# Optimization experiments

Measured on AMD Instinct MI355X. Metric: run time of the kernel, lower is better.

## Reference

```python
import jax, jax.numpy as jnp
import numpy as np

CUTOFF = 10.0
EPS_W = 1e-5
EPS_LN = 1e-5

def _silu(v):
    return v * jax.nn.sigmoid(v)

def setup_inputs() -> dict:
    key = jax.random.key(0)
    ks = jax.random.split(key, 12)
    N, E, H, R = 50000, 300000, 256, 64
    s = lambda fan_in: 1.0 / np.sqrt(fan_in)
    inp = {
        'x': jax.random.normal(ks[0], (N, H), jnp.float32),
        'edge_index': jax.random.randint(ks[1], (2, E), 0, N, jnp.int64 if jax.config.jax_enable_x64 else jnp.int32),
        'distances': jax.random.uniform(ks[2], (E,), jnp.float32) * CUTOFF,
        'centers': jnp.linspace(0.0, CUTOFF, R).astype(jnp.float32),
        'widths': jnp.full((R,), CUTOFF / R, jnp.float32),
        'rbf_w1': jax.random.normal(ks[3], (R, R), jnp.float32) * s(R),
        'rbf_b1': jnp.zeros((R,), jnp.float32),
        'rbf_w2': jax.random.normal(ks[4], (R, R), jnp.float32) * s(R),
        'rbf_b2': jnp.zeros((R,), jnp.float32),
        'filt_w1': jax.random.normal(ks[5], (R, H), jnp.float32) * s(R),
        'filt_b1': jnp.zeros((H,), jnp.float32),
        'filt_w2': jax.random.normal(ks[6], (H, H), jnp.float32) * s(H),
        'filt_b2': jnp.zeros((H,), jnp.float32),
        'filt_w3': jax.random.normal(ks[7], (H, H), jnp.float32) * s(H),
        'filt_b3': jnp.zeros((H,), jnp.float32),
        'node_w': jax.random.normal(ks[8], (H, H), jnp.float32) * s(H),
        'node_b': jnp.zeros((H,), jnp.float32),
        'ln_g': jnp.ones((H,), jnp.float32),
        'ln_b': jnp.zeros((H,), jnp.float32),
        'gate_w': jax.random.normal(ks[9], (H, H), jnp.float32) * s(H),
        'gate_b': jnp.zeros((H,), jnp.float32),
    }
    return inp

def reference(x, edge_index, distances, centers, widths,
              rbf_w1, rbf_b1, rbf_w2, rbf_b2,
              filt_w1, filt_b1, filt_w2, filt_b2, filt_w3, filt_b3,
              node_w, node_b, ln_g, ln_b, gate_w, gate_b):
    # LearnableRBF: envelope * gaussian basis, then 2-layer SiLU proj
    d = distances
    env = 0.5 * (jnp.cos(d * jnp.pi / CUTOFF) + 1.0) * (d < CUTOFF).astype(x.dtype)  # [E]
    rbf = jnp.exp(-0.5 * ((d[:, None] - centers) / (jnp.abs(widths) + EPS_W)) ** 2)   # [E,R]
    r = rbf * env[:, None]
    r = _silu(r @ rbf_w1 + rbf_b1) @ rbf_w2 + rbf_b2                                  # [E,R]
    # filter network: Lin-SiLU-Lin-SiLU-Lin
    W = _silu(r @ filt_w1 + filt_b1)
    W = _silu(W @ filt_w2 + filt_b2) @ filt_w3 + filt_b3                              # [E,H]
    # gather -> modulate -> scatter-add (CFConv messaging)
    row, col = edge_index[0], edge_index[1]
    msg = (x[col] @ node_w + node_b) * W                                              # [E,H]
    agg = jax.ops.segment_sum(msg, row, num_segments=x.shape[0])                      # [N,H]
    h = x + agg
    mu = jnp.mean(h, axis=-1, keepdims=True)
    var = jnp.var(h, axis=-1, keepdims=True)
    out = (h - mu) / jnp.sqrt(var + EPS_LN) * ln_g + ln_b
    return out * jax.nn.sigmoid(out @ gate_w + gate_b)
```

## Files before the change

kernel.cpp:

```cpp
#include <hip/hip_runtime.h>
#include <hip/hip_bf16.h>
#include <math.h>

typedef __attribute__((ext_vector_type(8))) short bf16x8;
typedef __attribute__((ext_vector_type(4))) float f32x4;
typedef unsigned short ushort_t;

constexpr float F_CUTOFF = 10.0f;
constexpr float F_EPS_W  = 1e-5f;
constexpr float F_EPS_LN = 1e-5f;
constexpr float F_PI     = 3.14159265358979323846f;

__device__ __forceinline__ float silu_f(float v)   { return v / (1.0f + __expf(-v)); }
__device__ __forceinline__ float sigmoid_f(float v){ return 1.0f / (1.0f + __expf(-v)); }

__device__ __forceinline__ ushort_t f2bf(float f) {
    union { __hip_bfloat16 h; ushort_t u; } v; v.h = __float2bfloat16(f); return v.u;
}
__device__ __forceinline__ float bf2f(ushort_t u) {
    union { unsigned u; float f; } v; v.u = ((unsigned)u) << 16; return v.f;
}

__global__ void count_kernel(const int* __restrict__ eidx, int* __restrict__ cnt, int E)
{
    int e = blockIdx.x * 256 + threadIdx.x;
    if (e < E) atomicAdd(&cnt[eidx[e]], 1);
}

__global__ __launch_bounds__(256)
void scan_sum_kernel(const int* __restrict__ cnt, int* __restrict__ part, int N, int range)
{
    __shared__ int red[256];
    int base = blockIdx.x * range;
    int s = 0;
    for (int i = threadIdx.x; i < range; i += 256) {
        int idx = base + i;
        if (idx < N) s += cnt[idx];
    }
    red[threadIdx.x] = s;
    __syncthreads();
    #pragma unroll
    for (int o = 128; o > 0; o >>= 1) {
        if (threadIdx.x < o) red[threadIdx.x] += red[threadIdx.x + o];
        __syncthreads();
    }
    if (threadIdx.x == 0) part[blockIdx.x] = red[0];
}

__global__ __launch_bounds__(256)
void scan_write_kernel(const int* __restrict__ part, int* __restrict__ cnt ,
                       int* __restrict__ start, int N, int range, int E)
{
    __shared__ int ex[256];
    int tid = threadIdx.x;
    int v = part[tid];
    ex[tid] = v;
    __syncthreads();
    for (int o = 1; o < 256; o <<= 1) {
        int add = (tid >= o) ? ex[tid - o] : 0;
        __syncthreads();
        ex[tid] += add;
        __syncthreads();
    }
    int run = ex[tid] - v;
    int base = tid * range;
    for (int i = 0; i < range; ++i) {
        int idx = base + i;
        if (idx < N) {
            int c = cnt[idx];
            start[idx] = run;
            cnt[idx] = run;
            run += c;
        }
    }
    if (tid == 0) start[N] = E;
}

__global__ void scatter_kernel(const int* __restrict__ eidx, const float* __restrict__ dist,
                               int* __restrict__ cursor,
                               int* __restrict__ colp, int* __restrict__ nodep,
                               float* __restrict__ distp, int E)
{
    int e = blockIdx.x * 256 + threadIdx.x;
    if (e < E) {
        int row = eidx[e];
        int s = atomicAdd(&cursor[row], 1);
        colp[s]  = eidx[E + e];
        nodep[s] = row;
        distp[s] = dist[e];
    }
}

__global__ void cvt_transpose_kernel(const float* __restrict__ in, ushort_t* __restrict__ out,
                                     int K, int N, int logK)
{
    int idx = blockIdx.x * 256 + threadIdx.x;
    if (idx >= K * N) return;
    int n = idx >> logK;
    int k = idx & (K - 1);
    out[idx] = f2bf(in[k * N + n]);
}

__global__ void combine_w_kernel(const float* __restrict__ w2, const float* __restrict__ fw1,
                                 ushort_t* __restrict__ out)
{
    int idx = blockIdx.x * 256 + threadIdx.x;
    int c = idx >> 6, j = idx & 63;
    float s = 0.f;
    #pragma unroll 8
    for (int n = 0; n < 64; ++n) s += w2[j * 64 + n] * fw1[n * 256 + c];
    out[idx] = f2bf(s);
}

__global__ void combine_b_kernel(const float* __restrict__ b2, const float* __restrict__ fw1,
                                 const float* __restrict__ fb1, float* __restrict__ out)
{
    int c = threadIdx.x;
    float s = fb1[c];
    #pragma unroll 8
    for (int n = 0; n < 64; ++n) s += b2[n] * fw1[n * 256 + c];
    out[c] = s;
}

__global__ __launch_bounds__(256)
void gemm256_bf16_kernel(const float* __restrict__ A, const float* __restrict__ Wm,
                         const float* __restrict__ bias, ushort_t* __restrict__ out, int M)
{
    __shared__ float4 As4[64][64];
    const int t = threadIdx.x;
    const int row0 = blockIdx.x * 64;

    #pragma unroll
    for (int i = 0; i < 16; ++i) {
        int flat = t + i * 256;
        int r = flat >> 6, k4 = flat & 63;
        int row = row0 + r;
        float4 v = make_float4(0.f, 0.f, 0.f, 0.f);
        if (row < M) v = reinterpret_cast<const float4*>(A)[row * 64 + k4];
        As4[r][k4] = v;
    }
    __syncthreads();

    const int jt  = t & 31;
    const int et  = t >> 5;
    const int j04 = jt * 2;
    const int r0  = et * 8;

    float acc[8][8];
    #pragma unroll
    for (int r = 0; r < 8; ++r)
        #pragma unroll
        for (int c = 0; c < 8; ++c) acc[r][c] = 0.f;

    for (int k4 = 0; k4 < 64; ++k4) {
        float4 a4[8];
        #pragma unroll
        for (int r = 0; r < 8; ++r) a4[r] = As4[r0 + r][k4];
        #pragma unroll
        for (int q = 0; q < 4; ++q) {
            const int k = k4 * 4 + q;
            float4 b0 = reinterpret_cast<const float4*>(Wm)[k * 64 + j04];
            float4 b1 = reinterpret_cast<const float4*>(Wm)[k * 64 + j04 + 1];
            float bb[8] = {b0.x, b0.y, b0.z, b0.w, b1.x, b1.y, b1.z, b1.w};
            float av;
            #pragma unroll
            for (int r = 0; r < 8; ++r) {
                av = (q == 0) ? a4[r].x : (q == 1) ? a4[r].y : (q == 2) ? a4[r].z : a4[r].w;
                #pragma unroll
                for (int c = 0; c < 8; ++c) acc[r][c] = fmaf(av, bb[c], acc[r][c]);
            }
        }
    }

    float4 bv0 = reinterpret_cast<const float4*>(bias)[j04];
    float4 bv1 = reinterpret_cast<const float4*>(bias)[j04 + 1];
    float bb[8] = {bv0.x, bv0.y, bv0.z, bv0.w, bv1.x, bv1.y, bv1.z, bv1.w};

    #pragma unroll
    for (int r = 0; r < 8; ++r) {
        int row = row0 + r0 + r;
        if (row >= M) continue;
        ushort_t o8[8];
        #pragma unroll
        for (int c = 0; c < 8; ++c) o8[c] = f2bf(acc[r][c] + bb[c]);
        *reinterpret_cast<uint4*>(out + (size_t)row * 256 + jt * 8) = *reinterpret_cast<uint4*>(o8);
    }
}

__global__ __launch_bounds__(256)
void gate_gemm_kernel(const float* __restrict__ A, const float* __restrict__ Wm,
                      const float* __restrict__ bias, float* __restrict__ out, int M)
{
    __shared__ float4 As4[64][64];
    const int t = threadIdx.x;
    const int row0 = blockIdx.x * 64;

    #pragma unroll
    for (int i = 0; i < 16; ++i) {
        int flat = t + i * 256;
        int r = flat >> 6, k4 = flat & 63;
        int row = row0 + r;
        float4 v = make_float4(0.f, 0.f, 0.f, 0.f);
        if (row < M) v = reinterpret_cast<const float4*>(A)[row * 64 + k4];
        As4[r][k4] = v;
    }
    __syncthreads();

    const int jt  = t & 31;
    const int et  = t >> 5;
    const int j04 = jt * 2;
    const int r0  = et * 8;

    float acc[8][8];
    #pragma unroll
    for (int r = 0; r < 8; ++r)
        #pragma unroll
        for (int c = 0; c < 8; ++c) acc[r][c] = 0.f;

    for (int k4 = 0; k4 < 64; ++k4) {
        float4 a4[8];
        #pragma unroll
        for (int r = 0; r < 8; ++r) a4[r] = As4[r0 + r][k4];
        #pragma unroll
        for (int q = 0; q < 4; ++q) {
            const int k = k4 * 4 + q;
            float4 b0 = reinterpret_cast<const float4*>(Wm)[k * 64 + j04];
            float4 b1 = reinterpret_cast<const float4*>(Wm)[k * 64 + j04 + 1];
            float bb[8] = {b0.x, b0.y, b0.z, b0.w, b1.x, b1.y, b1.z, b1.w};
            float av;
            #pragma unroll
            for (int r = 0; r < 8; ++r) {
                av = (q == 0) ? a4[r].x : (q == 1) ? a4[r].y : (q == 2) ? a4[r].z : a4[r].w;
                #pragma unroll
                for (int c = 0; c < 8; ++c) acc[r][c] = fmaf(av, bb[c], acc[r][c]);
            }
        }
    }

    float4 bv0 = reinterpret_cast<const float4*>(bias)[j04];
    float4 bv1 = reinterpret_cast<const float4*>(bias)[j04 + 1];
    float bb[8] = {bv0.x, bv0.y, bv0.z, bv0.w, bv1.x, bv1.y, bv1.z, bv1.w};

    #pragma unroll
    for (int r = 0; r < 8; ++r) {
        int row = row0 + r0 + r;
        if (row >= M) continue;
        float4 a0 = As4[r0 + r][j04];
        float4 a1 = As4[r0 + r][j04 + 1];
        float aa[8] = {a0.x, a0.y, a0.z, a0.w, a1.x, a1.y, a1.z, a1.w};
        float o[8];
        #pragma unroll
        for (int c = 0; c < 8; ++c) o[c] = aa[c] * sigmoid_f(acc[r][c] + bb[c]);
        reinterpret_cast<float4*>(out)[row * 64 + j04]     = make_float4(o[0], o[1], o[2], o[3]);
        reinterpret_cast<float4*>(out)[row * 64 + j04 + 1] = make_float4(o[4], o[5], o[6], o[7]);
    }
}

__global__ __launch_bounds__(256)
void rbf_kernel(const float* __restrict__ distp,
                const float* __restrict__ centers, const float* __restrict__ widths,
                ushort_t* __restrict__ r, int Mc)
{
    int idx = blockIdx.x * 256 + threadIdx.x;
    if (idx >= Mc * 8) return;
    int e  = idx >> 3;
    int c0 = (idx & 7) * 8;
    float d = distp[e];
    float env = (d < F_CUTOFF) ? 0.5f * (__cosf(d * (F_PI / F_CUTOFF)) + 1.0f) : 0.0f;
    ushort_t o[8];
    #pragma unroll
    for (int i = 0; i < 8; ++i) {
        int n = c0 + i;
        float w = fabsf(widths[n]) + F_EPS_W;
        float z = (d - centers[n]) / w;
        o[i] = f2bf(env * __expf(-0.5f * z * z));
    }
    *reinterpret_cast<uint4*>(r + (size_t)e * 64 + c0) = *reinterpret_cast<uint4*>(o);
}

__global__ __launch_bounds__(256, 4)
void gemm_k64_kernel(const ushort_t* A, const ushort_t* __restrict__ Wt,
                     const float* __restrict__ bias, ushort_t* out, int M)
{
    __shared__ __align__(16) unsigned char sA[128 * 128];
    const int t = threadIdx.x;
    const int m0 = blockIdx.x * 128;
    const int w = t >> 6, lane = t & 63;
    const int g = lane >> 4, q = lane & 15;

    #pragma unroll
    for (int i = 0; i < 4; ++i) {
        int s = t + i * 256;
        int r = s >> 3, u = s & 7;
        int row = m0 + r; row = (row < M) ? row : (M - 1);
        uint4 v = *reinterpret_cast<const uint4*>(A + (size_t)row * 64 + ((u ^ (r & 7)) * 8));
        *reinterpret_cast<uint4*>(sA + s * 16) = v;
    }
    __syncthreads();

    f32x4 acc[2][4];
    #pragma unroll
    for (int mt = 0; mt < 2; ++mt)
        #pragma unroll
        for (int nt = 0; nt < 4; ++nt) acc[mt][nt] = (f32x4){0.f, 0.f, 0.f, 0.f};

    #pragma unroll
    for (int kk = 0; kk < 2; ++kk) {
        bf16x8 b[4];
        #pragma unroll
        for (int nt = 0; nt < 4; ++nt) {
            int n = nt * 16 + q;
            b[nt] = *reinterpret_cast<const bf16x8*>(Wt + n * 64 + kk * 32 + g * 8);
        }
        bf16x8 a[2];
        #pragma unroll
        for (int mt = 0; mt < 2; ++mt) {
            int m = w * 32 + mt * 16 + q;
            int unit = (4 * kk + g) ^ (m & 7);
            a[mt] = *reinterpret_cast<const bf16x8*>(sA + m * 128 + unit * 16);
        }
        #pragma unroll
        for (int mt = 0; mt < 2; ++mt)
            #pragma unroll
            for (int nt = 0; nt < 4; ++nt)
                acc[mt][nt] = __builtin_amdgcn_mfma_f32_16x16x32_bf16(a[mt], b[nt], acc[mt][nt], 0, 0, 0);
    }
    __syncthreads();

    const bool evenq = (q & 1) == 0;
    #pragma unroll
    for (int nt = 0; nt < 4; ++nt) {
        int n0  = nt * 16 + q;
        int n_e = n0 & ~1;
        float2 bv = *reinterpret_cast<const float2*>(bias + n_e);
        #pragma unroll
        for (int mt = 0; mt < 2; ++mt) {
            float v[4], p[4];
            #pragma unroll
            for (int r = 0; r < 4; ++r) { v[r] = acc[mt][nt][r]; p[r] = __shfl_xor(v[r], 1, 64); }
            #pragma unroll
            for (int rr = 0; rr < 2; ++rr) {
                int r = evenq ? rr : (2 + rr);
                float lo = silu_f((evenq ? v[r] : p[r]) + bv.x);
                float hi = silu_f((evenq ? p[r] : v[r]) + bv.y);
                int m = w * 32 + mt * 16 + 4 * g + r;
                unsigned u = (unsigned)f2bf(lo) | ((unsigned)f2bf(hi) << 16);
                *reinterpret_cast<unsigned*>(sA + m * 128 + n_e * 2) = u;
            }
        }
    }
    __syncthreads();

    {
        int row = t >> 1, j = t & 1;
        if (m0 + row < M) {
            #pragma unroll
            for (int i = 0; i < 4; ++i) {
                uint4 v = *reinterpret_cast<const uint4*>(sA + row * 128 + (j * 4 + i) * 16);
                *reinterpret_cast<uint4*>(out + (size_t)(m0 + row) * 64 + (j * 4 + i) * 8) = v;
            }
        }
    }
}

__global__ __launch_bounds__(256, 4)
void gemm_k64n256_kernel(const ushort_t* __restrict__ A, const ushort_t* __restrict__ Wt,
                         const float* __restrict__ bias, ushort_t* __restrict__ out, int M)
{
    __shared__ __align__(16) unsigned char sA[64 * 128];
    __shared__ __align__(16) unsigned char obuf[32 * 512];
    const int t = threadIdx.x;
    const int m0 = blockIdx.x * 64;
    const int wn = t >> 6, lane = t & 63;
    const int g = lane >> 4, q = lane & 15;

    #pragma unroll
    for (int i = 0; i < 2; ++i) {
        int s = t + i * 256;
        int r = s >> 3, u = s & 7;
        int row = m0 + r; row = (row < M) ? row : (M - 1);
        uint4 v = *reinterpret_cast<const uint4*>(A + (size_t)row * 64 + ((u ^ (r & 7)) * 8));
        *reinterpret_cast<uint4*>(sA + s * 16) = v;
    }
    __syncthreads();

    f32x4 acc[4][4];
    #pragma unroll
    for (int mt = 0; mt < 4; ++mt)
        #pragma unroll
        for (int nt = 0; nt < 4; ++nt) acc[mt][nt] = (f32x4){0.f, 0.f, 0.f, 0.f};

    #pragma unroll
    for (int kk = 0; kk < 2; ++kk) {
        bf16x8 b[4];
        #pragma unroll
        for (int nt = 0; nt < 4; ++nt) {
            int n = wn * 64 + nt * 16 + q;
            b[nt] = *reinterpret_cast<const bf16x8*>(Wt + n * 64 + kk * 32 + g * 8);
        }
        bf16x8 a[4];
        #pragma unroll
        for (int mt = 0; mt < 4; ++mt) {
            int m = mt * 16 + q;
            int unit = (4 * kk + g) ^ (m & 7);
            a[mt] = *reinterpret_cast<const bf16x8*>(sA + m * 128 + unit * 16);
        }
        #pragma unroll
        for (int mt = 0; mt < 4; ++mt)
            #pragma unroll
            for (int nt = 0; nt < 4; ++nt)
                acc[mt][nt] = __builtin_amdgcn_mfma_f32_16x16x32_bf16(a[mt], b[nt], acc[mt][nt], 0, 0, 0);
    }

    const bool evenq = (q & 1) == 0;
    #pragma unroll
    for (int half = 0; half < 2; ++half) {
        #pragma unroll
        for (int mtl = 0; mtl < 2; ++mtl) {
            int mt = half * 2 + mtl;
            #pragma unroll
            for (int nt = 0; nt < 4; ++nt) {
                int n0  = wn * 64 + nt * 16 + q;
                int n_e = n0 & ~1;
                float2 bv = *reinterpret_cast<const float2*>(bias + n_e);
                float v[4], p[4];
                #pragma unroll
                for (int r = 0; r < 4; ++r) { v[r] = acc[mt][nt][r]; p[r] = __shfl_xor(v[r], 1, 64); }
                #pragma unroll
                for (int rr = 0; rr < 2; ++rr) {
                    int r = evenq ? rr : (2 + rr);
                    float lo = silu_f((evenq ? v[r] : p[r]) + bv.x);
                    float hi = silu_f((evenq ? p[r] : v[r]) + bv.y);
                    int ml = mtl * 16 + 4 * g + r;
                    unsigned u = (unsigned)f2bf(lo) | ((unsigned)f2bf(hi) << 16);
                    *reinterpret_cast<unsigned*>(obuf + ml * 512 + n_e * 2) = u;
                }
            }
        }
        __syncthreads();
        {
            int row = t >> 3, c = t & 7;
            int grow = m0 + half * 32 + row;
            if (grow < M) {
                #pragma unroll
                for (int i = 0; i < 4; ++i) {
                    uint4 v = *reinterpret_cast<const uint4*>(obuf + row * 512 + (c + 8 * i) * 16);
                    *reinterpret_cast<uint4*>(out + (size_t)grow * 256 + (c + 8 * i) * 8) = v;
                }
            }
        }
        __syncthreads();
    }
}

__global__ __launch_bounds__(256, 3)
void fused_de_kernel(const ushort_t* A, const ushort_t* __restrict__ Wt2,
                     const float* __restrict__ b2,
                     const ushort_t* __restrict__ Wt3, const float* __restrict__ b3,
                     ushort_t* out, int M)
{
    __shared__ __align__(16) unsigned char sbuf[2][8192];
    __shared__ __align__(16) unsigned char f2l[64 * 512];

    const int t  = threadIdx.x;
    const int m0 = blockIdx.x * 64;
    const int wn   = t >> 6;
    const int lane = t & 63;
    const int g = lane >> 4, q = lane & 15;

    const int s0r = t >> 3,         s0u = t & 7;
    const int s1r = (t + 256) >> 3, s1u = t & 7;
    const ushort_t* src0base = A + (size_t)((m0 + s0r < M) ? (m0 + s0r) : (M - 1)) * 256 + ((s0u ^ (s0r & 7)) * 8);
    const ushort_t* src1base = A + (size_t)((m0 + s1r < M) ? (m0 + s1r) : (M - 1)) * 256 + ((s1u ^ (s1r & 7)) * 8);

    uint4 p0 = *reinterpret_cast<const uint4*>(src0base);
    uint4 p1 = *reinterpret_cast<const uint4*>(src1base);
    *reinterpret_cast<uint4*>(&sbuf[0][t * 16])         = p0;
    *reinterpret_cast<uint4*>(&sbuf[0][(t + 256) * 16]) = p1;
    __syncthreads();

    f32x4 acc[4][4];
    #pragma unroll
    for (int mt = 0; mt < 4; ++mt)
        #pragma unroll
        for (int nt = 0; nt < 4; ++nt) acc[mt][nt] = (f32x4){0.f, 0.f, 0.f, 0.f};

    for (int kt = 0; kt < 4; ++kt) {
        const int cur = kt & 1;
        uint4 nx0, nx1;
        if (kt < 3) {
            nx0 = *reinterpret_cast<const uint4*>(src0base + (kt + 1) * 64);
            nx1 = *reinterpret_cast<const uint4*>(src1base + (kt + 1) * 64);
        }
        #pragma unroll
        for (int ks = 0; ks < 2; ++ks) {
            bf16x8 b[4];
            #pragma unroll
            for (int nt = 0; nt < 4; ++nt) {
                int n = wn * 64 + nt * 16 + q;
                b[nt] = *reinterpret_cast<const bf16x8*>(Wt2 + (size_t)n * 256 + kt * 64 + ks * 32 + g * 8);
            }
            bf16x8 a[4];
            #pragma unroll
            for (int mt = 0; mt < 4; ++mt) {
                int r = mt * 16 + q;
                int u = (ks * 4 + g) ^ (r & 7);
                a[mt] = *reinterpret_cast<const bf16x8*>(&sbuf[cur][r * 128 + u * 16]);
            }
            #pragma unroll
            for (int mt = 0; mt < 4; ++mt)
                #pragma unroll
                for (int nt = 0; nt < 4; ++nt)
                    acc[mt][nt] = __builtin_amdgcn_mfma_f32_16x16x32_bf16(a[mt], b[nt], acc[mt][nt], 0, 0, 0);
        }
        __syncthreads();
        if (kt < 3) {
            *reinterpret_cast<uint4*>(&sbuf[cur ^ 1][t * 16])         = nx0;
            *reinterpret_cast<uint4*>(&sbuf[cur ^ 1][(t + 256) * 16]) = nx1;
            __syncthreads();
        }
    }

    const bool evenq = (q & 1) == 0;
    #pragma unroll
    for (int nt = 0; nt < 4; ++nt) {
        int n0  = wn * 64 + nt * 16 + q;
        int n_e = n0 & ~1;
        float2 bv = *reinterpret_cast<const float2*>(b2 + n_e);
        #pragma unroll
        for (int mt = 0; mt < 4; ++mt) {
            float v[4], p[4];
            #pragma unroll
            for (int r = 0; r < 4; ++r) { v[r] = acc[mt][nt][r]; p[r] = __shfl_xor(v[r], 1, 64); }
            #pragma unroll
            for (int rr = 0; rr < 2; ++rr) {
                int r = evenq ? rr : (2 + rr);
                float lo = silu_f((evenq ? v[r] : p[r]) + bv.x);
                float hi = silu_f((evenq ? p[r] : v[r]) + bv.y);
                int m = mt * 16 + 4 * g + r;
                unsigned u = (unsigned)f2bf(lo) | ((unsigned)f2bf(hi) << 16);
                int byte = m * 512 + (((n_e >> 3) ^ (m & 7)) << 4) + ((n_e & 7) * 2);
                *reinterpret_cast<unsigned*>(f2l + byte) = u;
            }
        }
    }
    __syncthreads();

    #pragma unroll
    for (int mt = 0; mt < 4; ++mt)
        #pragma unroll
        for (int nt = 0; nt < 4; ++nt) acc[mt][nt] = (f32x4){0.f, 0.f, 0.f, 0.f};

    #pragma unroll
    for (int kk = 0; kk < 8; ++kk) {
        bf16x8 b[4];
        #pragma unroll
        for (int nt = 0; nt < 4; ++nt) {
            int n = wn * 64 + nt * 16 + q;
            b[nt] = *reinterpret_cast<const bf16x8*>(Wt3 + (size_t)n * 256 + kk * 32 + g * 8);
        }
        bf16x8 a[4];
        #pragma unroll
        for (int mt = 0; mt < 4; ++mt) {
            int m = mt * 16 + q;
            int unit = (4 * kk + g) ^ (m & 7);
            a[mt] = *reinterpret_cast<const bf16x8*>(f2l + m * 512 + unit * 16);
        }
        #pragma unroll
        for (int mt = 0; mt < 4; ++mt)
            #pragma unroll
            for (int nt = 0; nt < 4; ++nt)
                acc[mt][nt] = __builtin_amdgcn_mfma_f32_16x16x32_bf16(a[mt], b[nt], acc[mt][nt], 0, 0, 0);
    }

    unsigned char* obuf = &sbuf[0][0];
    #pragma unroll
    for (int half = 0; half < 2; ++half) {
        __syncthreads();
        #pragma unroll
        for (int mtl = 0; mtl < 2; ++mtl) {
            int mt = half * 2 + mtl;
            #pragma unroll
            for (int nt = 0; nt < 4; ++nt) {
                int n0  = wn * 64 + nt * 16 + q;
                int n_e = n0 & ~1;
                float2 bv = *reinterpret_cast<const float2*>(b3 + n_e);
                float v[4], p[4];
                #pragma unroll
                for (int r = 0; r < 4; ++r) { v[r] = acc[mt][nt][r]; p[r] = __shfl_xor(v[r], 1, 64); }
                #pragma unroll
                for (int rr = 0; rr < 2; ++rr) {
                    int r = evenq ? rr : (2 + rr);
                    float lo = (evenq ? v[r] : p[r]) + bv.x;
                    float hi = (evenq ? p[r] : v[r]) + bv.y;
                    int ml = mtl * 16 + 4 * g + r;
                    unsigned u = (unsigned)f2bf(lo) | ((unsigned)f2bf(hi) << 16);
                    *reinterpret_cast<unsigned*>(obuf + ml * 512 + n_e * 2) = u;
                }
            }
        }
        __syncthreads();
        {
            int row = t >> 3, c = t & 7;
            int grow = m0 + half * 32 + row;
            if (grow < M) {
                #pragma unroll
                for (int i = 0; i < 4; ++i) {
                    uint4 v = *reinterpret_cast<const uint4*>(obuf + row * 512 + (c + 8 * i) * 16);
                    *reinterpret_cast<uint4*>(out + (size_t)grow * 256 + (c + 8 * i) * 8) = v;
                }
            }
        }
    }
}

__global__ __launch_bounds__(256)
void agg_node_kernel(const ushort_t* __restrict__ Wf, const int* __restrict__ colp,
                     const int* __restrict__ start, const ushort_t* __restrict__ y,
                     float* __restrict__ agg, int cs, int ce, int N)
{
    int lane = threadIdx.x & 63;
    int n    = blockIdx.x * 4 + (threadIdx.x >> 6);
    if (n >= N) return;
    int s0 = start[n], s1 = start[n + 1];
    if (s1 <= cs || s0 >= ce) return;
    int lo = (s0 > cs) ? s0 : cs;
    int hi = (s1 < ce) ? s1 : ce;

    float h0 = 0.f, h1 = 0.f, h2 = 0.f, h3 = 0.f;
    for (int s = lo; s < hi; ++s) {
        uint2 wv = *reinterpret_cast<const uint2*>(Wf + (size_t)(s - cs) * 256 + lane * 4);
        int c = colp[s];
        uint2 yv = *reinterpret_cast<const uint2*>(y + (size_t)c * 256 + lane * 4);
        h0 += bf2f((ushort_t)(wv.x & 0xffff)) * bf2f((ushort_t)(yv.x & 0xffff));
        h1 += bf2f((ushort_t)(wv.x >> 16))    * bf2f((ushort_t)(yv.x >> 16));
        h2 += bf2f((ushort_t)(wv.y & 0xffff)) * bf2f((ushort_t)(yv.y & 0xffff));
        h3 += bf2f((ushort_t)(wv.y >> 16))    * bf2f((ushort_t)(yv.y >> 16));
    }

    float* row = agg + (size_t)n * 256 + lane * 4;
    if (s0 >= cs && s1 <= ce) {
        *reinterpret_cast<float4*>(row) = make_float4(h0, h1, h2, h3);
    } else {
        unsafeAtomicAdd(&row[0], h0);
        unsafeAtomicAdd(&row[1], h1);
        unsafeAtomicAdd(&row[2], h2);
        unsafeAtomicAdd(&row[3], h3);
    }
}

template<int KS, int NT, bool SILU>
__device__ __forceinline__ void mlp_stage(const unsigned char* in, unsigned char* out,
                                          const ushort_t* __restrict__ Wt,
                                          const float* __restrict__ bias,
                                          int wn, int g, int q)
{
    constexpr int K = KS * 32;
    f32x4 acc[2][NT];
    #pragma unroll
    for (int mt = 0; mt < 2; ++mt)
        #pragma unroll
        for (int nt = 0; nt < NT; ++nt) acc[mt][nt] = (f32x4){0.f, 0.f, 0.f, 0.f};

    #pragma unroll
    for (int kk = 0; kk < KS; ++kk) {
        bf16x8 b[NT];
        #pragma unroll
        for (int nt = 0; nt < NT; ++nt) {
            int n = (wn * NT + nt) * 16 + q;
            b[nt] = *reinterpret_cast<const bf16x8*>(Wt + n * K + kk * 32 + g * 8);
        }
        bf16x8 a[2];
        #pragma unroll
        for (int mt = 0; mt < 2; ++mt) {
            int m = mt * 16 + q;
            int unit = (4 * kk + g) ^ (m & 7);
            a[mt] = *reinterpret_cast<const bf16x8*>(in + m * 512 + unit * 16);
        }
        #pragma unroll
        for (int mt = 0; mt < 2; ++mt)
            #pragma unroll
            for (int nt = 0; nt < NT; ++nt)
                acc[mt][nt] = __builtin_amdgcn_mfma_f32_16x16x32_bf16(a[mt], b[nt], acc[mt][nt], 0, 0, 0);
    }

    const bool evenq = (q & 1) == 0;
    #pragma unroll
    for (int nt = 0; nt < NT; ++nt) {
        int n0  = (wn * NT + nt) * 16 + q;
        int n_e = n0 & ~1;
        float2 bv = *reinterpret_cast<const float2*>(bias + n_e);
        #pragma unroll
        for (int mt = 0; mt < 2; ++mt) {
            float v[4], p[4];
            #pragma unroll
            for (int r = 0; r < 4; ++r) { v[r] = acc[mt][nt][r]; p[r] = __shfl_xor(v[r], 1, 64); }
            #pragma unroll
            for (int rr = 0; rr < 2; ++rr) {
                int r = evenq ? rr : (2 + rr);
                float lo = (evenq ? v[r] : p[r]) + bv.x;
                float hi = (evenq ? p[r] : v[r]) + bv.y;
                if (SILU) { lo = silu_f(lo); hi = silu_f(hi); }
                int m = mt * 16 + 4 * g + r;
                unsigned u = (unsigned)f2bf(lo) | ((unsigned)f2bf(hi) << 16);
                int byte = m * 512 + (((n_e >> 3) ^ (m & 7)) << 4) + ((n_e & 7) * 2);
                *reinterpret_cast<unsigned*>(out + byte) = u;
            }
        }
    }
}

__global__ __launch_bounds__(256, 4)
void edge_csr_kernel(const float* __restrict__ distp, const int* __restrict__ colp,
                     const int* __restrict__ nodep, const int* __restrict__ start,
                     const float* __restrict__ centers, const float* __restrict__ widths,
                     const ushort_t* __restrict__ wt_rbf1, const float* __restrict__ rbf_b1,
                     const ushort_t* __restrict__ wt_comb, const float* __restrict__ b_comb,
                     const ushort_t* __restrict__ wt_f2, const float* __restrict__ filt_b2,
                     const ushort_t* __restrict__ wt_f3, const float* __restrict__ filt_b3,
                     const ushort_t* __restrict__ y, float* __restrict__ agg, int E)
{
    __shared__ __align__(16) unsigned char buf[32768];
    __shared__ int node_s[32];
    __shared__ int flag_s[32];
    unsigned char* bufA = buf;
    unsigned char* bufB = buf + 16384;

    const int t  = threadIdx.x;
    const int e0 = blockIdx.x * 32;
    const int wn   = t >> 6;
    const int lane = t & 63;
    const int g = lane >> 4, q = lane & 15;

    if (t < 32) {
        int ge = e0 + t;
        int nd = (ge < E) ? nodep[ge] : -1;
        node_s[t] = nd;
        int fl = 0;
        if (nd >= 0) {
            int lo = start[nd], hi = start[nd + 1];
            fl = (lo >= e0 && hi <= e0 + 32) ? 1 : 0;
        }
        flag_s[t] = fl;
    }

    const int e_own  = t >> 3;
    const int chunk  = t & 7;
    const int ge_own = e0 + e_own;
    const int col_own = (ge_own < E) ? colp[ge_own] : 0;
    uint4 yv[4];
    #pragma unroll
    for (int i = 0; i < 4; ++i)
        yv[i] = *reinterpret_cast<const uint4*>(y + (size_t)col_own * 256 + (i * 8 + chunk) * 8);

    {
        float d = (ge_own < E) ? distp[ge_own] : F_CUTOFF;
        float env = (d < F_CUTOFF) ? 0.5f * (__cosf(d * (F_PI / F_CUTOFF)) + 1.0f) : 0.0f;
        unsigned char* rowp = bufA + e_own * 512;
        int k0 = chunk * 8;
        #pragma unroll
        for (int i = 0; i < 4; ++i) {
            int n = k0 + 2 * i;
            float c0 = centers[n],     w0 = fabsf(widths[n]) + F_EPS_W;
            float c1 = centers[n + 1], w1 = fabsf(widths[n + 1]) + F_EPS_W;
            float z0 = (d - c0) / w0, z1 = (d - c1) / w1;
            float r0 = env * __expf(-0.5f * z0 * z0);
            float r1 = env * __expf(-0.5f * z1 * z1);
            unsigned u = (unsigned)f2bf(r0) | ((unsigned)f2bf(r1) << 16);
            int byte = (((n >> 3) ^ (e_own & 7)) << 4) + ((n & 7) * 2);
            *reinterpret_cast<unsigned*>(rowp + byte) = u;
        }
    }
    __syncthreads();

    mlp_stage<2, 1, true>(bufA, bufB, wt_rbf1, rbf_b1, wn, g, q);
    __syncthreads();
    mlp_stage<2, 4, true>(bufB, bufA, wt_comb, b_comb, wn, g, q);
    __syncthreads();
    mlp_stage<8, 4, true>(bufA, bufB, wt_f2, filt_b2, wn, g, q);
    __syncthreads();

    #pragma unroll
    for (int i = 0; i < 4; ++i)
        *reinterpret_cast<uint4*>(bufA + e_own * 512 + (i * 8 + chunk) * 16) = yv[i];
    __syncthreads();

    f32x4 acc[2][4];
    #pragma unroll
    for (int mt = 0; mt < 2; ++mt)
        #pragma unroll
        for (int nt = 0; nt < 4; ++nt) acc[mt][nt] = (f32x4){0.f, 0.f, 0.f, 0.f};

    #pragma unroll
    for (int kk = 0; kk < 8; ++kk) {
        bf16x8 b[4];
        #pragma unroll
        for (int nt = 0; nt < 4; ++nt) {
            int n = (wn * 4 + nt) * 16 + q;
            b[nt] = *reinterpret_cast<const bf16x8*>(wt_f3 + n * 256 + kk * 32 + g * 8);
        }
        bf16x8 a[2];
        #pragma unroll
        for (int mt = 0; mt < 2; ++mt) {
            int m = mt * 16 + q;
            int unit = (4 * kk + g) ^ (m & 7);
            a[mt] = *reinterpret_cast<const bf16x8*>(bufB + m * 512 + unit * 16);
        }
        #pragma unroll
        for (int mt = 0; mt < 2; ++mt)
            #pragma unroll
            for (int nt = 0; nt < 4; ++nt)
                acc[mt][nt] = __builtin_amdgcn_mfma_f32_16x16x32_bf16(a[mt], b[nt], acc[mt][nt], 0, 0, 0);
    }

    float bn[4];
    int   nn[4];
    #pragma unroll
    for (int nt = 0; nt < 4; ++nt) { nn[nt] = (wn * 4 + nt) * 16 + q; bn[nt] = filt_b3[nn[nt]]; }

    #pragma unroll
    for (int mt = 0; mt < 2; ++mt) {
        #pragma unroll
        for (int r = 0; r < 4; ++r) {
            int m = mt * 16 + 4 * g + r;
            const unsigned char* yrow = bufA + m * 512;
            #pragma unroll
            for (int nt = 0; nt < 4; ++nt) {
                float yvv = bf2f(*reinterpret_cast<const ushort_t*>(yrow + nn[nt] * 2));
                acc[mt][nt][r] = (acc[mt][nt][r] + bn[nt]) * yvv;
            }
        }
    }
    __syncthreads();

    float* msgf = reinterpret_cast<float*>(buf);
    #pragma unroll
    for (int mt = 0; mt < 2; ++mt) {
        #pragma unroll
        for (int r = 0; r < 4; ++r) {
            int m = mt * 16 + 4 * g + r;
            #pragma unroll
            for (int nt = 0; nt < 4; ++nt)
                msgf[m * 256 + nn[nt]] = acc[mt][nt][r];
        }
    }
    __syncthreads();

    {
        const int j = t;
        float accv = 0.f;
        int cur = -2, rs = 0;
        #pragma unroll 4
        for (int r = 0; r < 32; ++r) {
            int nd = node_s[r];
            if (nd != cur) {
                if (cur >= 0) {
                    if (flag_s[rs]) agg[(size_t)cur * 256 + j] = accv;
                    else            unsafeAtomicAdd(&agg[(size_t)cur * 256 + j], accv);
                }
                cur = nd; rs = r; accv = msgf[r * 256 + j];
            } else {
                accv += msgf[r * 256 + j];
            }
        }
        if (cur >= 0) {
            if (flag_s[rs]) agg[(size_t)cur * 256 + j] = accv;
            else            unsafeAtomicAdd(&agg[(size_t)cur * 256 + j], accv);
        }
    }
}

__global__ __launch_bounds__(256)
void ln_kernel(const float* __restrict__ x, const float* __restrict__ agg,
               const float* __restrict__ g, const float* __restrict__ b,
               float* __restrict__ out0, int N)
{
    int lane = threadIdx.x & 63;
    int row  = blockIdx.x * 4 + (threadIdx.x >> 6);
    if (row >= N) return;
    float4 hx = reinterpret_cast<const float4*>(x)[row * 64 + lane];
    float4 ha = reinterpret_cast<const float4*>(agg)[row * 64 + lane];
    float4 h  = make_float4(hx.x + ha.x, hx.y + ha.y, hx.z + ha.z, hx.w + ha.w);
    float s  = h.x + h.y + h.z + h.w;
    float s2 = h.x * h.x + h.y * h.y + h.z * h.z + h.w * h.w;
    #pragma unroll
    for (int off = 32; off > 0; off >>= 1) {
        s  += __shfl_xor(s,  off, 64);
        s2 += __shfl_xor(s2, off, 64);
    }
    float mu  = s * (1.0f / 256.0f);
    float var = s2 * (1.0f / 256.0f) - mu * mu;
    float inv = rsqrtf(var + F_EPS_LN);
    float4 gv = reinterpret_cast<const float4*>(g)[lane];
    float4 bv = reinterpret_cast<const float4*>(b)[lane];
    float4 o;
    o.x = (h.x - mu) * inv * gv.x + bv.x;
    o.y = (h.y - mu) * inv * gv.y + bv.y;
    o.z = (h.z - mu) * inv * gv.z + bv.z;
    o.w = (h.w - mu) * inv * gv.w + bv.w;
    reinterpret_cast<float4*>(out0)[row * 64 + lane] = o;
}

extern "C" void kernel_launch(void* const* d_in, const int* in_sizes, int n_in,
                              void* d_out, int out_size, void* d_ws, size_t ws_size,
                              hipStream_t stream)
{
    const float* x       = (const float*)d_in[0];
    const int*   eidx    = (const int*)  d_in[1];
    const float* dist    = (const float*)d_in[2];
    const float* centers = (const float*)d_in[3];
    const float* widths  = (const float*)d_in[4];
    const float* rbf_w1  = (const float*)d_in[5];
    const float* rbf_b1  = (const float*)d_in[6];
    const float* rbf_w2  = (const float*)d_in[7];
    const float* rbf_b2  = (const float*)d_in[8];
    const float* filt_w1 = (const float*)d_in[9];
    const float* filt_b1 = (const float*)d_in[10];
    const float* filt_w2 = (const float*)d_in[11];
    const float* filt_b2 = (const float*)d_in[12];
    const float* filt_w3 = (const float*)d_in[13];
    const float* filt_b3 = (const float*)d_in[14];
    const float* node_w  = (const float*)d_in[15];
    const float* node_b  = (const float*)d_in[16];
    const float* ln_g    = (const float*)d_in[17];
    const float* ln_b    = (const float*)d_in[18];
    const float* gate_w  = (const float*)d_in[19];
    const float* gate_b  = (const float*)d_in[20];

    const int N = in_sizes[0] / 256;
    const int E = in_sizes[2];

    char* wsb = (char*)d_ws;
    size_t off = 0;
    auto alloc = [&](size_t bytes, size_t align) -> char* {
        off = (off + align - 1) & ~(align - 1);
        char* p = wsb + off;
        off += bytes;
        return p;
    };
    ushort_t* y_bf  = (ushort_t*)alloc((size_t)N * 256 * 2, 16);
    ushort_t* wt1   = (ushort_t*)alloc(64 * 64 * 2, 16);
    ushort_t* wcomb = (ushort_t*)alloc(256 * 64 * 2, 16);
    ushort_t* wf2t  = (ushort_t*)alloc(256 * 256 * 2, 16);
    ushort_t* wf3t  = (ushort_t*)alloc(256 * 256 * 2, 16);
    float*    bcomb = (float*)   alloc(256 * 4, 16);
    int*      part  = (int*)     alloc(256 * 4, 16);
    int*      cnt   = (int*)     alloc((size_t)N * 4, 16);
    int*      start = (int*)     alloc(((size_t)N + 1) * 4, 16);
    int*      colp  = (int*)     alloc((size_t)E * 4, 16);
    int*      nodep = (int*)     alloc((size_t)E * 4, 16);
    float*    distp = (float*)   alloc((size_t)E * 4, 256);

    size_t fixed_off = (off + 1023) & ~(size_t)1023;
    size_t avail = (ws_size > fixed_off) ? (ws_size - fixed_off) : 0;
    long Rl = (long)(avail / 640);
    int R = (int)(Rl & ~127L);
    int Eround = (E + 127) & ~127;
    if (R > Eround) R = Eround;
    const bool dense = (R >= 128) && ((E + R - 1) / R <= 8);
    ushort_t* rt_buf = (ushort_t*)(wsb + fixed_off);
    ushort_t* fw_buf = rt_buf + (size_t)R * 64;

    dim3 b256(256);
    const int range = (N + 255) / 256;

    cvt_transpose_kernel<<<dim3((64 * 64 + 255) / 256),   b256, 0, stream>>>(rbf_w1,  wt1, 64, 64, 6);
    combine_w_kernel<<<dim3(64), b256, 0, stream>>>(rbf_w2, filt_w1, wcomb);
    combine_b_kernel<<<dim3(1), b256, 0, stream>>>(rbf_b2, filt_w1, filt_b1, bcomb);
    cvt_transpose_kernel<<<dim3((256 * 256 + 255) / 256), b256, 0, stream>>>(filt_w2, wf2t, 256, 256, 8);
    cvt_transpose_kernel<<<dim3((256 * 256 + 255) / 256), b256, 0, stream>>>(filt_w3, wf3t, 256, 256, 8);

    gemm256_bf16_kernel<<<dim3((N + 63) / 64), b256, 0, stream>>>(x, node_w, node_b, y_bf, N);

    hipMemsetAsync(d_out, 0, (size_t)out_size * sizeof(float), stream);
    hipMemsetAsync(cnt, 0, (size_t)N * 4, stream);

    count_kernel<<<dim3((E + 255) / 256), b256, 0, stream>>>(eidx, cnt, E);
    scan_sum_kernel<<<dim3(256), b256, 0, stream>>>(cnt, part, N, range);
    scan_write_kernel<<<dim3(1), b256, 0, stream>>>(part, cnt, start, N, range, E);
    scatter_kernel<<<dim3((E + 255) / 256), b256, 0, stream>>>(eidx, dist, cnt, colp, nodep, distp, E);

    if (dense) {
        for (int cs = 0; cs < E; cs += R) {
            int Mc = (E - cs < R) ? (E - cs) : R;
            rbf_kernel<<<dim3((Mc * 8 + 255) / 256), b256, 0, stream>>>(
                distp + cs, centers, widths, rt_buf, Mc);
            gemm_k64_kernel<<<dim3((Mc + 127) / 128), b256, 0, stream>>>(
                rt_buf, wt1, rbf_b1, rt_buf, Mc);
            gemm_k64n256_kernel<<<dim3((Mc + 63) / 64), b256, 0, stream>>>(
                rt_buf, wcomb, bcomb, fw_buf, Mc);
            fused_de_kernel<<<dim3((Mc + 63) / 64), b256, 0, stream>>>(
                fw_buf, wf2t, filt_b2, wf3t, filt_b3, fw_buf, Mc);
            agg_node_kernel<<<dim3((N + 3) / 4), b256, 0, stream>>>(
                fw_buf, colp, start, y_bf, (float*)d_out, cs, cs + Mc, N);
        }
    } else {
        edge_csr_kernel<<<dim3((E + 31) / 32), b256, 0, stream>>>(
            distp, colp, nodep, start, centers, widths,
            wt1, rbf_b1, wcomb, bcomb,
            wf2t, filt_b2, wf3t, filt_b3,
            y_bf, (float*)d_out, E);
    }

    ln_kernel<<<dim3((N + 3) / 4), b256, 0, stream>>>(x, (float*)d_out, ln_g, ln_b, (float*)d_out, N);
    gate_gemm_kernel<<<dim3((N + 63) / 64), b256, 0, stream>>>((float*)d_out, gate_w, gate_b, (float*)d_out, N);
}
```

Measured before the change: 984.1 us.

## Use bf16 MFMA GEMMs for node projection and gate on dense path

Replaces the fp32 node projection GEMM and the gate GEMM with bf16 MFMA kernels on the dense path. x is first cast to bf16, and the LayerNorm kernel also writes a bf16 copy of its output for the gate GEMM. Both bf16 copies reuse the chunk workspace, so dense mode is now also gated on the workspace being large enough for an N×256 bf16 buffer. The aim is to move two N×256×256 GEMMs onto matrix cores, at the cost of extra cast traffic and lower input precision for the gate.

```diff
diff --git a/kernel.cpp b/kernel.cpp
--- a/kernel.cpp
+++ b/kernel.cpp
@@ -123,6 +123,16 @@
 }
 
 __global__ __launch_bounds__(256)
+void cast_bf16_kernel(const float* __restrict__ in, ushort_t* __restrict__ out, long n4)
+{
+    long i = (long)blockIdx.x * 256 + threadIdx.x;
+    if (i >= n4) return;
+    float4 v = reinterpret_cast<const float4*>(in)[i];
+    ushort_t o[4] = {f2bf(v.x), f2bf(v.y), f2bf(v.z), f2bf(v.w)};
+    *reinterpret_cast<uint2*>(out + i * 4) = *reinterpret_cast<uint2*>(o);
+}
+
+__global__ __launch_bounds__(256)
 void gemm256_bf16_kernel(const float* __restrict__ A, const float* __restrict__ Wm,
                          const float* __restrict__ bias, ushort_t* __restrict__ out, int M)
 {
@@ -446,6 +456,215 @@
                 for (int i = 0; i < 4; ++i) {
                     uint4 v = *reinterpret_cast<const uint4*>(obuf + row * 512 + (c + 8 * i) * 16);
                     *reinterpret_cast<uint4*>(out + (size_t)grow * 256 + (c + 8 * i) * 8) = v;
+                }
+            }
+        }
+        __syncthreads();
+    }
+}
+
+template<bool SILU>
+__global__ __launch_bounds__(256, 3)
+void gemm_k256_kernel(const ushort_t* __restrict__ A, const ushort_t* __restrict__ Wt,
+                      const float* __restrict__ bias, ushort_t* __restrict__ out, int M)
+{
+    __shared__ __align__(16) unsigned char sbuf[2][8192];
+
+    const int t  = threadIdx.x;
+    const int m0 = blockIdx.x * 64;
+    const int wn   = t >> 6;
+    const int lane = t & 63;
+    const int g = lane >> 4, q = lane & 15;
+
+    const int s0r = t >> 3,         s0u = t & 7;
+    const int s1r = (t + 256) >> 3, s1u = t & 7;
+    const ushort_t* src0base = A + (size_t)((m0 + s0r < M) ? (m0 + s0r) : (M - 1)) * 256 + ((s0u ^ (s0r & 7)) * 8);
+    const ushort_t* src1base = A + (size_t)((m0 + s1r < M) ? (m0 + s1r) : (M - 1)) * 256 + ((s1u ^ (s1r & 7)) * 8);
+
+    uint4 p0 = *reinterpret_cast<const uint4*>(src0base);
+    uint4 p1 = *reinterpret_cast<const uint4*>(src1base);
+    *reinterpret_cast<uint4*>(&sbuf[0][t * 16])         = p0;
+    *reinterpret_cast<uint4*>(&sbuf[0][(t + 256) * 16]) = p1;
+    __syncthreads();
+
+    f32x4 acc[4][4];
+    #pragma unroll
+    for (int mt = 0; mt < 4; ++mt)
+        #pragma unroll
+        for (int nt = 0; nt < 4; ++nt) acc[mt][nt] = (f32x4){0.f, 0.f, 0.f, 0.f};
+
+    for (int kt = 0; kt < 4; ++kt) {
+        const int cur = kt & 1;
+        uint4 nx0, nx1;
+        if (kt < 3) {
+            nx0 = *reinterpret_cast<const uint4*>(src0base + (kt + 1) * 64);
+            nx1 = *reinterpret_cast<const uint4*>(src1base + (kt + 1) * 64);
+        }
+        #pragma unroll
+        for (int ks = 0; ks < 2; ++ks) {
+            bf16x8 b[4];
+            #pragma unroll
+            for (int nt = 0; nt < 4; ++nt) {
+                int n = wn * 64 + nt * 16 + q;
+                b[nt] = *reinterpret_cast<const bf16x8*>(Wt + (size_t)n * 256 + kt * 64 + ks * 32 + g * 8);
+            }
+            bf16x8 a[4];
+            #pragma unroll
+            for (int mt = 0; mt < 4; ++mt) {
+                int r = mt * 16 + q;
+                int u = (ks * 4 + g) ^ (r & 7);
+                a[mt] = *reinterpret_cast<const bf16x8*>(&sbuf[cur][r * 128 + u * 16]);
+            }
+            #pragma unroll
+            for (int mt = 0; mt < 4; ++mt)
+                #pragma unroll
+                for (int nt = 0; nt < 4; ++nt)
+                    acc[mt][nt] = __builtin_amdgcn_mfma_f32_16x16x32_bf16(a[mt], b[nt], acc[mt][nt], 0, 0, 0);
+        }
+        __syncthreads();
+        if (kt < 3) {
+            *reinterpret_cast<uint4*>(&sbuf[cur ^ 1][t * 16])         = nx0;
+            *reinterpret_cast<uint4*>(&sbuf[cur ^ 1][(t + 256) * 16]) = nx1;
+            __syncthreads();
+        }
+    }
+
+    unsigned char* obuf = &sbuf[0][0];
+    const bool evenq = (q & 1) == 0;
+    #pragma unroll
+    for (int half = 0; half < 2; ++half) {
+        __syncthreads();
+        #pragma unroll
+        for (int mtl = 0; mtl < 2; ++mtl) {
+            int mt = half * 2 + mtl;
+            #pragma unroll
+            for (int nt = 0; nt < 4; ++nt) {
+                int n0  = wn * 64 + nt * 16 + q;
+                int n_e = n0 & ~1;
+                float2 bv = *reinterpret_cast<const float2*>(bias + n_e);
+                float v[4], p[4];
+                #pragma unroll
+                for (int r = 0; r < 4; ++r) { v[r] = acc[mt][nt][r]; p[r] = __shfl_xor(v[r], 1, 64); }
+                #pragma unroll
+                for (int rr = 0; rr < 2; ++rr) {
+                    int r = evenq ? rr : (2 + rr);
+                    float lo = (evenq ? v[r] : p[r]) + bv.x;
+                    float hi = (evenq ? p[r] : v[r]) + bv.y;
+                    if (SILU) { lo = silu_f(lo); hi = silu_f(hi); }
+                    int ml = mtl * 16 + 4 * g + r;
+                    unsigned u = (unsigned)f2bf(lo) | ((unsigned)f2bf(hi) << 16);
+                    *reinterpret_cast<unsigned*>(obuf + ml * 512 + n_e * 2) = u;
+                }
+            }
+        }
+        __syncthreads();
+        {
+            int row = t >> 3, c = t & 7;
+            int grow = m0 + half * 32 + row;
+            if (grow < M) {
+                #pragma unroll
+                for (int i = 0; i < 4; ++i) {
+                    uint4 v = *reinterpret_cast<const uint4*>(obuf + row * 512 + (c + 8 * i) * 16);
+                    *reinterpret_cast<uint4*>(out + (size_t)grow * 256 + (c + 8 * i) * 8) = v;
+                }
+            }
+        }
+    }
+}
+
+__global__ __launch_bounds__(256, 4)
+void gate_mfma_kernel(const ushort_t* __restrict__ A, const ushort_t* __restrict__ Wt,
+                      const float* __restrict__ bias, float* __restrict__ out, int M)
+{
+    __shared__ __align__(16) unsigned char sbuf[2][8192];
+    __shared__ float obuf[16][260];
+
+    const int t  = threadIdx.x;
+    const int m0 = blockIdx.x * 64;
+    const int wn   = t >> 6;
+    const int lane = t & 63;
+    const int g = lane >> 4, q = lane & 15;
+
+    const int s0r = t >> 3,         s0u = t & 7;
+    const int s1r = (t + 256) >> 3, s1u = t & 7;
+    const ushort_t* src0base = A + (size_t)((m0 + s0r < M) ? (m0 + s0r) : (M - 1)) * 256 + ((s0u ^ (s0r & 7)) * 8);
+    const ushort_t* src1base = A + (size_t)((m0 + s1r < M) ? (m0 + s1r) : (M - 1)) * 256 + ((s1u ^ (s1r & 7)) * 8);
+
+    uint4 p0 = *reinterpret_cast<const uint4*>(src0base);
+    uint4 p1 = *reinterpret_cast<const uint4*>(src1base);
+    *reinterpret_cast<uint4*>(&sbuf[0][t * 16])         = p0;
+    *reinterpret_cast<uint4*>(&sbuf[0][(t + 256) * 16]) = p1;
+    __syncthreads();
+
+    f32x4 acc[4][4];
+    #pragma unroll
+    for (int mt = 0; mt < 4; ++mt)
+        #pragma unroll
+        for (int nt = 0; nt < 4; ++nt) acc[mt][nt] = (f32x4){0.f, 0.f, 0.f, 0.f};
+
+    for (int kt = 0; kt < 4; ++kt) {
+        const int cur = kt & 1;
+        uint4 nx0, nx1;
+        if (kt < 3) {
+            nx0 = *reinterpret_cast<const uint4*>(src0base + (kt + 1) * 64);
+            nx1 = *reinterpret_cast<const uint4*>(src1base + (kt + 1) * 64);
+        }
+        #pragma unroll
+        for (int ks = 0; ks < 2; ++ks) {
+            bf16x8 b[4];
+            #pragma unroll
+            for (int nt = 0; nt < 4; ++nt) {
+                int n = wn * 64 + nt * 16 + q;
+                b[nt] = *reinterpret_cast<const bf16x8*>(Wt + (size_t)n * 256 + kt * 64 + ks * 32 + g * 8);
+            }
+            bf16x8 a[4];
+            #pragma unroll
+            for (int mt = 0; mt < 4; ++mt) {
+                int r = mt * 16 + q;
+                int u = (ks * 4 + g) ^ (r & 7);
+                a[mt] = *reinterpret_cast<const bf16x8*>(&sbuf[cur][r * 128 + u * 16]);
+            }
+            #pragma unroll
+            for (int mt = 0; mt < 4; ++mt)
+                #pragma unroll
+                for (int nt = 0; nt < 4; ++nt)
+                    acc[mt][nt] = __builtin_amdgcn_mfma_f32_16x16x32_bf16(a[mt], b[nt], acc[mt][nt], 0, 0, 0);
+        }
+        __syncthreads();
+        if (kt < 3) {
+            *reinterpret_cast<uint4*>(&sbuf[cur ^ 1][t * 16])         = nx0;
+            *reinterpret_cast<uint4*>(&sbuf[cur ^ 1][(t + 256) * 16]) = nx1;
+            __syncthreads();
+        }
+    }
+
+    float bn[4];
+    #pragma unroll
+    for (int nt = 0; nt < 4; ++nt) bn[nt] = bias[wn * 64 + nt * 16 + q];
+
+    #pragma unroll
+    for (int p = 0; p < 4; ++p) {
+        #pragma unroll
+        for (int nt = 0; nt < 4; ++nt) {
+            int col = wn * 64 + nt * 16 + q;
+            #pragma unroll
+            for (int r = 0; r < 4; ++r) {
+                int rl = 4 * g + r;
+                obuf[rl][col] = sigmoid_f(acc[p][nt][r] + bn[nt]);
+            }
+        }
+        __syncthreads();
+        {
+            int rl = t >> 4, c16 = t & 15;
+            int grow = m0 + p * 16 + rl;
+            if (grow < M) {
+                float* orow = out + (size_t)grow * 256 + c16 * 16;
+                #pragma unroll
+                for (int i = 0; i < 4; ++i) {
+                    float4 g4 = *reinterpret_cast<const float4*>(&obuf[rl][c16 * 16 + i * 4]);
+                    float4 a4 = *reinterpret_cast<const float4*>(orow + i * 4);
+                    a4.x *= g4.x; a4.y *= g4.y; a4.z *= g4.z; a4.w *= g4.w;
+                    *reinterpret_cast<float4*>(orow + i * 4) = a4;
                 }
             }
         }
@@ -873,7 +1092,7 @@
 __global__ __launch_bounds__(256)
 void ln_kernel(const float* __restrict__ x, const float* __restrict__ agg,
                const float* __restrict__ g, const float* __restrict__ b,
-               float* __restrict__ out0, int N)
+               float* __restrict__ out0, ushort_t* __restrict__ out_bf, int N)
 {
     int lane = threadIdx.x & 63;
     int row  = blockIdx.x * 4 + (threadIdx.x >> 6);
@@ -899,6 +1118,8 @@
     o.z = (h.z - mu) * inv * gv.z + bv.z;
     o.w = (h.w - mu) * inv * gv.w + bv.w;
     reinterpret_cast<float4*>(out0)[row * 64 + lane] = o;
+    ushort_t ob[4] = {f2bf(o.x), f2bf(o.y), f2bf(o.z), f2bf(o.w)};
+    *reinterpret_cast<uint2*>(out_bf + (size_t)row * 256 + lane * 4) = *reinterpret_cast<uint2*>(ob);
 }
 
 extern "C" void kernel_launch(void* const* d_in, const int* in_sizes, int n_in,
@@ -938,18 +1159,20 @@
         off += bytes;
         return p;
     };
-    ushort_t* y_bf  = (ushort_t*)alloc((size_t)N * 256 * 2, 16);
-    ushort_t* wt1   = (ushort_t*)alloc(64 * 64 * 2, 16);
-    ushort_t* wcomb = (ushort_t*)alloc(256 * 64 * 2, 16);
-    ushort_t* wf2t  = (ushort_t*)alloc(256 * 256 * 2, 16);
-    ushort_t* wf3t  = (ushort_t*)alloc(256 * 256 * 2, 16);
-    float*    bcomb = (float*)   alloc(256 * 4, 16);
-    int*      part  = (int*)     alloc(256 * 4, 16);
-    int*      cnt   = (int*)     alloc((size_t)N * 4, 16);
-    int*      start = (int*)     alloc(((size_t)N + 1) * 4, 16);
-    int*      colp  = (int*)     alloc((size_t)E * 4, 16);
-    int*      nodep = (int*)     alloc((size_t)E * 4, 16);
-    float*    distp = (float*)   alloc((size_t)E * 4, 256);
+    ushort_t* y_bf   = (ushort_t*)alloc((size_t)N * 256 * 2, 16);
+    ushort_t* wt1    = (ushort_t*)alloc(64 * 64 * 2, 16);
+    ushort_t* wcomb  = (ushort_t*)alloc(256 * 64 * 2, 16);
+    ushort_t* wf2t   = (ushort_t*)alloc(256 * 256 * 2, 16);
+    ushort_t* wf3t   = (ushort_t*)alloc(256 * 256 * 2, 16);
+    ushort_t* wnodet = (ushort_t*)alloc(256 * 256 * 2, 16);
+    ushort_t* wgatet = (ushort_t*)alloc(256 * 256 * 2, 16);
+    float*    bcomb  = (float*)   alloc(256 * 4, 16);
+    int*      part   = (int*)     alloc(256 * 4, 16);
+    int*      cnt    = (int*)     alloc((size_t)N * 4, 16);
+    int*      start  = (int*)     alloc(((size_t)N + 1) * 4, 16);
+    int*      colp   = (int*)     alloc((size_t)E * 4, 16);
+    int*      nodep  = (int*)     alloc((size_t)E * 4, 16);
+    float*    distp  = (float*)   alloc((size_t)E * 4, 256);
 
     size_t fixed_off = (off + 1023) & ~(size_t)1023;
     size_t avail = (ws_size > fixed_off) ? (ws_size - fixed_off) : 0;
@@ -957,9 +1180,12 @@
     int R = (int)(Rl & ~127L);
     int Eround = (E + 127) & ~127;
     if (R > Eround) R = Eround;
-    const bool dense = (R >= 128) && ((E + R - 1) / R <= 8);
+    const bool dense = (R >= 128) && ((E + R - 1) / R <= 8)
+                       && ((size_t)R * 640 >= (size_t)N * 512 + 1024);
     ushort_t* rt_buf = (ushort_t*)(wsb + fixed_off);
     ushort_t* fw_buf = rt_buf + (size_t)R * 64;
+    ushort_t* x_bf   = rt_buf;
+    ushort_t* a_bf   = rt_buf;
 
     dim3 b256(256);
     const int range = (N + 255) / 256;
@@ -969,11 +1195,19 @@
     combine_b_kernel<<<dim3(1), b256, 0, stream>>>(rbf_b2, filt_w1, filt_b1, bcomb);
     cvt_transpose_kernel<<<dim3((256 * 256 + 255) / 256), b256, 0, stream>>>(filt_w2, wf2t, 256, 256, 8);
     cvt_transpose_kernel<<<dim3((256 * 256 + 255) / 256), b256, 0, stream>>>(filt_w3, wf3t, 256, 256, 8);
-
-    gemm256_bf16_kernel<<<dim3((N + 63) / 64), b256, 0, stream>>>(x, node_w, node_b, y_bf, N);
+    cvt_transpose_kernel<<<dim3((256 * 256 + 255) / 256), b256, 0, stream>>>(node_w,  wnodet, 256, 256, 8);
+    cvt_transpose_kernel<<<dim3((256 * 256 + 255) / 256), b256, 0, stream>>>(gate_w,  wgatet, 256, 256, 8);
 
     hipMemsetAsync(d_out, 0, (size_t)out_size * sizeof(float), stream);
     hipMemsetAsync(cnt, 0, (size_t)N * 4, stream);
+
+    if (dense) {
+        cast_bf16_kernel<<<dim3((N * 64 + 255) / 256), b256, 0, stream>>>(x, x_bf, (long)N * 64);
+        gemm_k256_kernel<false><<<dim3((N + 63) / 64), b256, 0, stream>>>(
+            x_bf, wnodet, node_b, y_bf, N);
+    } else {
+        gemm256_bf16_kernel<<<dim3((N + 63) / 64), b256, 0, stream>>>(x, node_w, node_b, y_bf, N);
+    }
 
     count_kernel<<<dim3((E + 255) / 256), b256, 0, stream>>>(eidx, cnt, E);
     scan_sum_kernel<<<dim3(256), b256, 0, stream>>>(cnt, part, N, range);
@@ -994,14 +1228,19 @@
             agg_node_kernel<<<dim3((N + 3) / 4), b256, 0, stream>>>(
                 fw_buf, colp, start, y_bf, (float*)d_out, cs, cs + Mc, N);
         }
+        ln_kernel<<<dim3((N + 3) / 4), b256, 0, stream>>>(
+            x, (float*)d_out, ln_g, ln_b, (float*)d_out, a_bf, N);
+        gate_mfma_kernel<<<dim3((N + 63) / 64), b256, 0, stream>>>(
+            a_bf, wgatet, gate_b, (float*)d_out, N);
     } else {
         edge_csr_kernel<<<dim3((E + 31) / 32), b256, 0, stream>>>(
             distp, colp, nodep, start, centers, widths,
             wt1, rbf_b1, wcomb, bcomb,
             wf2t, filt_b2, wf3t, filt_b3,
             y_bf, (float*)d_out, E);
-    }
-
-    ln_kernel<<<dim3((N + 3) / 4), b256, 0, stream>>>(x, (float*)d_out, ln_g, ln_b, (float*)d_out, N);
-    gate_gemm_kernel<<<dim3((N + 63) / 64), b256, 0, stream>>>((float*)d_out, gate_w, gate_b, (float*)d_out, N);
-}
+        ln_kernel<<<dim3((N + 3) / 4), b256, 0, stream>>>(
+            x, (float*)d_out, ln_g, ln_b, (float*)d_out, y_bf, N);
+        gate_gemm_kernel<<<dim3((N + 63) / 64), b256, 0, stream>>>(
+            (float*)d_out, gate_w, gate_b, (float*)d_out, N);
+    }
+}
```

Result: faster. 894.3 us (-9.1%).
